# Kernel optimization log

Measured on AMD Instinct MI355X. Metric: run time of the kernel, lower is better.

Reference implementation:

```python
import jax, jax.numpy as jnp
import numpy as np

WS = 8          # window size
NH = 12         # num heads
DEPTH = 2       # blocks: W-MSA, SW-MSA
EPS = 1e-6
N = WS * WS     # tokens per window


def _rel_index():
    c = np.stack(np.meshgrid(np.arange(WS), np.arange(WS), indexing='ij')).reshape(2, -1)
    rel = (c[:, :, None] - c[:, None, :]).transpose(1, 2, 0)
    rel[:, :, 0] += WS - 1
    rel[:, :, 1] += WS - 1
    rel[:, :, 0] *= 2 * WS - 1
    return rel.sum(-1)  # [N, N] int

REL_IDX = jnp.asarray(_rel_index())


def _shift_mask(H, W, shift):
    # static (numpy) construction, H/W/shift are Python ints
    img = np.zeros((H, W))
    cnt = 0
    for hs in (slice(0, -WS), slice(-WS, -shift), slice(-shift, None)):
        for wsl in (slice(0, -WS), slice(-WS, -shift), slice(-shift, None)):
            img[hs, wsl] = cnt
            cnt += 1
    win = img.reshape(H // WS, WS, W // WS, WS).transpose(0, 2, 1, 3).reshape(-1, N)
    diff = win[:, None, :] - win[:, :, None]
    return jnp.asarray(np.where(diff != 0, -100.0, 0.0), jnp.float32)  # [nW, N, N]


def _ln(x):
    m = x.mean(-1, keepdims=True)
    v = ((x - m) ** 2).mean(-1, keepdims=True)
    return (x - m) * jax.lax.rsqrt(v + EPS)


def _block(x, H, W, emb, p, shift):
    qkv_w, qkv_b, proj_w, proj_b, ff1_w, ff1_b, ff2_w, ff2_b, ada_w, ada_b, bias_table = p
    B, L, C = x.shape
    hd = C // NH
    ada = jax.nn.silu(emb) @ ada_w.T + ada_b  # [B, 6C]
    sh_sa, sc_sa, g_sa, sh_ff, sc_ff, g_ff = jnp.split(ada, 6, axis=-1)
    h = _ln(x) * (1.0 + sc_sa[:, None]) + sh_sa[:, None]
    h = h.reshape(B, H, W, C)
    if shift > 0:
        h = jnp.roll(h, (-shift, -shift), (1, 2))
    # window partition -> [B*nW, N, C]
    win = h.reshape(B, H // WS, WS, W // WS, WS, C).transpose(0, 1, 3, 2, 4, 5).reshape(-1, N, C)
    B_ = win.shape[0]
    qkv = (win @ qkv_w.T + qkv_b).reshape(B_, N, 3, NH, hd)
    q, k, v = qkv[:, :, 0], qkv[:, :, 1], qkv[:, :, 2]
    attn = jnp.einsum('bnhd,bmhd->bhnm', q, k) * (hd ** -0.5)
    bias = bias_table[REL_IDX]  # [N, N, NH]
    attn = attn + bias.transpose(2, 0, 1)[None]
    if shift > 0:
        mask = _shift_mask(H, W, shift)  # [nW, N, N]
        nW = mask.shape[0]
        attn = (attn.reshape(B, nW, NH, N, N) + mask[None, :, None]).reshape(B_, NH, N, N)
    attn = jax.nn.softmax(attn, axis=-1)
    out = jnp.einsum('bhnm,bmhd->bnhd', attn, v).reshape(B_, N, C)
    out = out @ proj_w.T + proj_b
    # window reverse
    h = out.reshape(B, H // WS, W // WS, WS, WS, C).transpose(0, 1, 3, 2, 4, 5).reshape(B, H, W, C)
    if shift > 0:
        h = jnp.roll(h, (shift, shift), (1, 2))
    x = x + g_sa[:, None] * h.reshape(B, L, C)
    h2 = _ln(x) * (1.0 + sc_ff[:, None]) + sh_ff[:, None]
    ff = jax.nn.gelu(h2 @ ff1_w.T + ff1_b, approximate=False) @ ff2_w.T + ff2_b
    return x + g_ff[:, None] * ff


def _forward(x, emb, H, W, params):
    for i in range(DEPTH):
        p = tuple(a[i] for a in params)
        x = _block(x, H, W, emb, p, 0 if i % 2 == 0 else WS // 2)
    return x


def setup_inputs() -> dict:
    key = jax.random.key(0)
    ks = jax.random.split(key, 16)
    C, E, FF = 384, 384, 4 * 384
    B, H, W = 8, 64, 64
    p = lambda k, shape: jax.random.normal(k, shape, jnp.float32) * 0.02
    return {
        'x': jax.random.normal(ks[0], (B, H * W, C), jnp.float32),
        'H': H,
        'W': W,
        'emb': jax.random.normal(ks[1], (B, E), jnp.float32),
        'qkv_w': p(ks[2], (DEPTH, 3 * C, C)),
        'qkv_b': p(ks[3], (DEPTH, 3 * C)),
        'proj_w': p(ks[4], (DEPTH, C, C)),
        'proj_b': p(ks[5], (DEPTH, C)),
        'ff1_w': p(ks[6], (DEPTH, FF, C)),
        'ff1_b': p(ks[7], (DEPTH, FF)),
        'ff2_w': p(ks[8], (DEPTH, C, FF)),
        'ff2_b': p(ks[9], (DEPTH, C)),
        'ada_w': p(ks[10], (DEPTH, 6 * C, E)),
        'ada_b': p(ks[11], (DEPTH, 6 * C)),
        'bias_table': p(ks[12], (DEPTH, (2 * WS - 1) ** 2, NH)),
    }


def reference(x, H, W, emb, qkv_w, qkv_b, proj_w, proj_b, ff1_w, ff1_b, ff2_w, ff2_b, ada_w, ada_b, bias_table):
    params = (qkv_w, qkv_b, proj_w, proj_b, ff1_w, ff1_b, ff2_w, ff2_b, ada_w, ada_b, bias_table)
    return _forward(x, emb, H, W, params)
```

## Files before the change

kernel.cpp:

```cpp
#include <hip/hip_runtime.h>

typedef __bf16 bf16_t;
typedef bf16_t bf16x8 __attribute__((ext_vector_type(8)));
typedef float f32x4 __attribute__((ext_vector_type(4)));

#define EPI_STORE 0
#define EPI_GELU 1
#define EPI_RES_WIN 2
#define EPI_RES_ID 3

__device__ __forceinline__ float bf2f(unsigned short u) {
    union { unsigned int i; float f; } x; x.i = ((unsigned int)u) << 16; return x.f;
}
__device__ __forceinline__ unsigned short f2bf(float f) {
    union { float f; unsigned int u; } x; x.f = f;
    unsigned int u = x.u;
    return (unsigned short)((u + 0x7fffu + ((u >> 16) & 1u)) >> 16);
}

__device__ __forceinline__ void async_cp16(const unsigned short* g, unsigned short* l) {
    __builtin_amdgcn_global_load_lds(
        (const __attribute__((address_space(1))) unsigned int*)g,
        (__attribute__((address_space(3))) unsigned int*)l, 16, 0, 0);
}

__device__ __forceinline__ int map_win(int m, int shift) {
    int n = m & 63, w = m >> 6;
    int b = w >> 6, ww = w & 63;
    int hh = ((ww >> 3) * 8 + (n >> 3) + shift) & 63;
    int wc = ((ww & 7) * 8 + (n & 7) + shift) & 63;
    return (b << 12) + (hh << 6) + wc;
}


__global__ void f2bf_kernel(const float* __restrict__ in,
                            unsigned short* __restrict__ out, int n) {
    int i = blockIdx.x * 256 + threadIdx.x;
    if (i < n) out[i] = f2bf(in[i]);
}

__global__ void silu_kernel(const float* __restrict__ emb,
                            float* __restrict__ out, int n) {
    int i = blockIdx.x * 256 + threadIdx.x;
    if (i < n) { float e = emb[i]; out[i] = e / (1.0f + expf(-e)); }
}

__global__ __launch_bounds__(64) void ada_kernel(
    const float* __restrict__ se,
    const float* __restrict__ ada_w,
    const float* __restrict__ ada_b,
    float* __restrict__ ada_out)
{
    int j = blockIdx.x;
    int layer = blockIdx.y;
    int t = threadIdx.x;
    const float* wr = ada_w + ((long)layer * 2304 + j) * 384;
    float w[6];
#pragma unroll
    for (int q = 0; q < 6; q++) w[q] = wr[t + 64 * q];
    float bias = ada_b[layer * 2304 + j];
    for (int b = 0; b < 8; b++) {
        float p = 0.f;
#pragma unroll
        for (int q = 0; q < 6; q++) p += se[b * 384 + t + 64 * q] * w[q];
#pragma unroll
        for (int o = 32; o > 0; o >>= 1) p += __shfl_xor(p, o);
        if (t == 0) ada_out[((long)layer * 8 + b) * 2304 + j] = p + bias;
    }
}

__global__ __launch_bounds__(256) void ln_mod_kernel(
    const float* __restrict__ x, const float* __restrict__ ada,
    unsigned short* __restrict__ h, int sh_off, int sc_off)
{
    int row = blockIdx.x * 4 + (threadIdx.x >> 6);
    int b = row >> 12;
    int t = threadIdx.x & 63;
    const float* xr = x + (long)row * 384;
    float v[6];
    float s = 0.f;
#pragma unroll
    for (int j = 0; j < 6; j++) { v[j] = xr[t + 64 * j]; s += v[j]; }
#pragma unroll
    for (int o = 32; o > 0; o >>= 1) s += __shfl_xor(s, o);
    float mean = s * (1.0f / 384.0f);
    float s2 = 0.f;
#pragma unroll
    for (int j = 0; j < 6; j++) { float d = v[j] - mean; s2 += d * d; }
#pragma unroll
    for (int o = 32; o > 0; o >>= 1) s2 += __shfl_xor(s2, o);
    float rstd = rsqrtf(s2 * (1.0f / 384.0f) + 1e-6f);
    const float* adab = ada + (long)b * 2304;
#pragma unroll
    for (int j = 0; j < 6; j++) {
        int c = t + 64 * j;
        float val = (v[j] - mean) * rstd * (1.0f + adab[sc_off + c]) + adab[sh_off + c];
        h[(long)row * 384 + c] = f2bf(val);
    }
}


template <int EPI, bool GATHER, bool RESINIT>
__global__ __launch_bounds__(256) void gemm128(
    const unsigned short* __restrict__ A,
    const unsigned short* __restrict__ W,
    const float* __restrict__ bias,
    unsigned short* __restrict__ out,
    float* __restrict__ xres,
    const float* __restrict__ xbase,
    const float* __restrict__ gvec,
    int M, int N, int K, int shift)
{
    __shared__ __align__(16) unsigned short As[128 * 32];
    __shared__ __align__(16) unsigned short Bs[128 * 32];

    const int tid = threadIdx.x;
    const int wv = tid >> 6, lane = tid & 63;
    const int m0 = blockIdx.y * 128, n0 = blockIdx.x * 128;

    const int srow = wv * 32 + (lane >> 2);
    const int scol = (lane & 3) * 8;
    const long asrc0 = GATHER ? (long)map_win(m0 + srow, shift) : (long)(m0 + srow);
    const long asrc1 = GATHER ? (long)map_win(m0 + srow + 16, shift) : (long)(m0 + srow + 16);
    const unsigned short* ag0 = A + asrc0 * K + scol;
    const unsigned short* ag1 = A + asrc1 * K + scol;
    const unsigned short* bg0 = W + (long)(n0 + srow) * K + scol;
    const unsigned short* bg1 = W + (long)(n0 + srow + 16) * K + scol;
    unsigned short* al0 = As + wv * 1024;
    unsigned short* al1 = As + wv * 1024 + 512;
    unsigned short* bl0 = Bs + wv * 1024;
    unsigned short* bl1 = Bs + wv * 1024 + 512;

    const int wm = (wv >> 1) * 64, wn = (wv & 1) * 64;
    const int l16 = lane & 15, quad = lane >> 4;

    f32x4 acc[4][4] = {};

    for (int k0 = 0; k0 < K; k0 += 32) {
        async_cp16(ag0 + k0, al0);
        async_cp16(ag1 + k0, al1);
        async_cp16(bg0 + k0, bl0);
        async_cp16(bg1 + k0, bl1);
        __syncthreads();

        bf16x8 af[4], bfr[4];
#pragma unroll
        for (int i = 0; i < 4; i++)
            af[i] = *(const bf16x8*)&As[(wm + i * 16 + l16) * 32 + quad * 8];
#pragma unroll
        for (int i = 0; i < 4; i++)
            bfr[i] = *(const bf16x8*)&Bs[(wn + i * 16 + l16) * 32 + quad * 8];
#pragma unroll
        for (int i = 0; i < 4; i++)
#pragma unroll
            for (int j = 0; j < 4; j++)
                acc[i][j] = __builtin_amdgcn_mfma_f32_16x16x32_bf16(af[i], bfr[j], acc[i][j], 0, 0, 0);
        __syncthreads();
    }

#pragma unroll
    for (int i = 0; i < 4; i++) {
#pragma unroll
        for (int j = 0; j < 4; j++) {
            int col = n0 + wn + j * 16 + l16;
            float bv = bias[col];
#pragma unroll
            for (int r = 0; r < 4; r++) {
                int row = m0 + wm + i * 16 + quad * 4 + r;
                float v = acc[i][j][r] + bv;
                if constexpr (EPI == EPI_STORE) {
                    out[(long)row * N + col] = f2bf(v);
                } else if constexpr (EPI == EPI_GELU) {
                    v = 0.5f * v * (1.0f + erff(v * 0.70710678118f));
                    out[(long)row * N + col] = f2bf(v);
                } else {
                    long dst = (EPI == EPI_RES_WIN) ? (long)map_win(row, shift) : (long)row;
                    int b = (int)(dst >> 12);
                    float g = gvec[(long)b * 2304 + col];
                    if constexpr (RESINIT)
                        xres[dst * 384 + col] = xbase[dst * 384 + col] + g * v;
                    else
                        xres[dst * 384 + col] += g * v;
                }
            }
        }
    }
}


__device__ __forceinline__ int reg3(int p) { return (p < 56) ? 0 : ((p < 60) ? 1 : 2); }

__global__ __launch_bounds__(256) void attn_kernel(
    const unsigned short* __restrict__ qkv,
    const float* __restrict__ bias_table,
    unsigned short* __restrict__ out,
    int shift)
{
    __shared__ unsigned short Pl[4][64 * 68];
    __shared__ unsigned short VTl[4][32 * 68];

    const int wv = threadIdx.x >> 6, lane = threadIdx.x & 63;
    const int head = blockIdx.x * 4 + wv;
    const int win = blockIdx.y;
    const int l16 = lane & 15, quad = lane >> 4;

    unsigned short* P = Pl[wv];
    unsigned short* vt = VTl[wv];

    const long base = (long)win * 64 * 1152 + head * 32;

    bf16x8 qf[4], kf[4];
#pragma unroll
    for (int i = 0; i < 4; i++) {
        qf[i] = *(const bf16x8*)&qkv[base + (long)(i * 16 + l16) * 1152 + quad * 8];
        kf[i] = *(const bf16x8*)&qkv[base + 384 + (long)(i * 16 + l16) * 1152 + quad * 8];
    }
    {
        const uint4* vp = (const uint4*)&qkv[base + 768 + (long)lane * 1152];
#pragma unroll
        for (int c4 = 0; c4 < 4; c4++) {
            uint4 v = vp[c4];
            unsigned int u[4] = {v.x, v.y, v.z, v.w};
#pragma unroll
            for (int e = 0; e < 4; e++) {
                vt[(c4 * 8 + e * 2) * 68 + lane]     = (unsigned short)(u[e] & 0xffffu);
                vt[(c4 * 8 + e * 2 + 1) * 68 + lane] = (unsigned short)(u[e] >> 16);
            }
        }
    }

    f32x4 sacc[4][4] = {};
#pragma unroll
    for (int i = 0; i < 4; i++)
#pragma unroll
        for (int j = 0; j < 4; j++)
            sacc[i][j] = __builtin_amdgcn_mfma_f32_16x16x32_bf16(qf[i], kf[j], sacc[i][j], 0, 0, 0);

    const float scale = 0.17677669529663687f;
    const int ww = win & 63, wi = ww >> 3, wj = ww & 7;

#pragma unroll
    for (int i = 0; i < 4; i++) {
#pragma unroll
        for (int r = 0; r < 4; r++) {
            int n = i * 16 + quad * 4 + r;
            int nr = n >> 3, nc = n & 7;
            int labq = (shift > 0) ? reg3(wi * 8 + nr) * 3 + reg3(wj * 8 + nc) : 0;
            float v[4];
#pragma unroll
            for (int j = 0; j < 4; j++) {
                int m = j * 16 + l16;
                int mr = m >> 3, mc = m & 7;
                float s = sacc[i][j][r] * scale +
                          bias_table[((nr - mr + 7) * 15 + (nc - mc + 7)) * 12 + head];
                if (shift > 0) {
                    int labm = reg3(wi * 8 + mr) * 3 + reg3(wj * 8 + mc);
                    if (labm != labq) s -= 100.0f;
                }
                v[j] = s;
            }
            float mx = fmaxf(fmaxf(v[0], v[1]), fmaxf(v[2], v[3]));
#pragma unroll
            for (int o = 1; o < 16; o <<= 1) mx = fmaxf(mx, __shfl_xor(mx, o));
            float sum = 0.f;
#pragma unroll
            for (int j = 0; j < 4; j++) { v[j] = __expf(v[j] - mx); sum += v[j]; }
#pragma unroll
            for (int o = 1; o < 16; o <<= 1) sum += __shfl_xor(sum, o);
            float inv = 1.0f / sum;
#pragma unroll
            for (int j = 0; j < 4; j++)
                P[n * 68 + j * 16 + l16] = f2bf(v[j] * inv);
        }
    }
    __syncthreads();

    f32x4 oacc[4][2] = {};
#pragma unroll
    for (int kt = 0; kt < 2; kt++) {
        bf16x8 pf[4], vf[2];
#pragma unroll
        for (int i = 0; i < 4; i++)
            pf[i] = *(const bf16x8*)&P[(i * 16 + l16) * 68 + kt * 32 + quad * 8];
#pragma unroll
        for (int jt = 0; jt < 2; jt++)
            vf[jt] = *(const bf16x8*)&vt[(jt * 16 + l16) * 68 + kt * 32 + quad * 8];
#pragma unroll
        for (int i = 0; i < 4; i++)
#pragma unroll
            for (int jt = 0; jt < 2; jt++)
                oacc[i][jt] = __builtin_amdgcn_mfma_f32_16x16x32_bf16(pf[i], vf[jt], oacc[i][jt], 0, 0, 0);
    }

#pragma unroll
    for (int i = 0; i < 4; i++)
#pragma unroll
        for (int jt = 0; jt < 2; jt++)
#pragma unroll
            for (int r = 0; r < 4; r++) {
                int row = i * 16 + quad * 4 + r;
                int col = jt * 16 + l16;
                out[((long)win * 64 + row) * 384 + head * 32 + col] = f2bf(oacc[i][jt][r]);
            }
}


extern "C" void kernel_launch(void* const* d_in, const int* in_sizes, int n_in,
                              void* d_out, int out_size, void* d_ws, size_t ws_size,
                              hipStream_t stream) {
    const float* x_in   = (const float*)d_in[0];
    const float* emb    = (const float*)d_in[3];
    const float* qkv_w  = (const float*)d_in[4];
    const float* qkv_b  = (const float*)d_in[5];
    const float* proj_w = (const float*)d_in[6];
    const float* proj_b = (const float*)d_in[7];
    const float* ff1_w  = (const float*)d_in[8];
    const float* ff1_b  = (const float*)d_in[9];
    const float* ff2_w  = (const float*)d_in[10];
    const float* ff2_b  = (const float*)d_in[11];
    const float* ada_w  = (const float*)d_in[12];
    const float* ada_b  = (const float*)d_in[13];
    const float* bias_t = (const float*)d_in[14];

    char* ws = (char*)d_ws;
    unsigned short* h_buf   = (unsigned short*)ws;
    unsigned short* big_buf = (unsigned short*)(ws + 25165824);
    unsigned short* wqkv    = (unsigned short*)(ws + 125829120);
    unsigned short* wproj   = (unsigned short*)(ws + 127598592);
    unsigned short* wff1    = (unsigned short*)(ws + 128188416);
    unsigned short* wff2    = (unsigned short*)(ws + 130547712);
    float*          ada_out = (float*)(ws + 132907008);
    float*          se      = (float*)(ws + 133054464);

    float* x_acc = (float*)d_out;

    const int M = 32768;

    f2bf_kernel<<<(884736 + 255) / 256, 256, 0, stream>>>(qkv_w, wqkv, 884736);
    f2bf_kernel<<<(294912 + 255) / 256, 256, 0, stream>>>(proj_w, wproj, 294912);
    f2bf_kernel<<<(1179648 + 255) / 256, 256, 0, stream>>>(ff1_w, wff1, 1179648);
    f2bf_kernel<<<(1179648 + 255) / 256, 256, 0, stream>>>(ff2_w, wff2, 1179648);

    silu_kernel<<<(3072 + 255) / 256, 256, 0, stream>>>(emb, se, 3072);
    ada_kernel<<<dim3(2304, 2), 64, 0, stream>>>(se, ada_w, ada_b, ada_out);

    for (int layer = 0; layer < 2; layer++) {
        const int shift = layer ? 4 : 0;
        const float* ada_l = ada_out + (long)layer * 8 * 2304;

        ln_mod_kernel<<<M / 4, 256, 0, stream>>>(layer == 0 ? x_in : x_acc,
                                                 ada_l, h_buf, 0, 384);

        gemm128<EPI_STORE, true, false><<<dim3(9, 256), 256, 0, stream>>>(
            h_buf, wqkv + (long)layer * 1152 * 384, qkv_b + layer * 1152,
            big_buf, nullptr, nullptr, nullptr, M, 1152, 384, shift);

        attn_kernel<<<dim3(3, 512), 256, 0, stream>>>(
            big_buf, bias_t + layer * 225 * 12, h_buf, shift);

        if (layer == 0) {
            gemm128<EPI_RES_WIN, false, true><<<dim3(3, 256), 256, 0, stream>>>(
                h_buf, wproj, proj_b,
                nullptr, x_acc, x_in, ada_l + 768, M, 384, 384, shift);
        } else {
            gemm128<EPI_RES_WIN, false, false><<<dim3(3, 256), 256, 0, stream>>>(
                h_buf, wproj + (long)384 * 384, proj_b + 384,
                nullptr, x_acc, nullptr, ada_l + 768, M, 384, 384, shift);
        }

        ln_mod_kernel<<<M / 4, 256, 0, stream>>>(x_acc, ada_l, h_buf, 1152, 1536);

        gemm128<EPI_GELU, false, false><<<dim3(12, 256), 256, 0, stream>>>(
            h_buf, wff1 + (long)layer * 1536 * 384, ff1_b + layer * 1536,
            big_buf, nullptr, nullptr, nullptr, M, 1536, 384, 0);

        gemm128<EPI_RES_ID, false, false><<<dim3(3, 256), 256, 0, stream>>>(
            big_buf, wff2 + (long)layer * 384 * 1536, ff2_b + layer * 384,
            nullptr, x_acc, nullptr, ada_l + 1920, M, 384, 1536, 0);
    }
}
```

Measured before the change: 794.8 us.

## Deepen GEMM K-tile to 64 with XOR-swizzled LDS, fast GELU and bf16 cast

Doubles the GEMM K-step to 64 so each shared-memory load and barrier pair covers twice the MFMA work. LDS tiles use an XOR swizzle on 16-byte chunks to avoid bank conflicts on the fragment reads. The erf-based GELU is replaced by a tanh-approximation written with __expf, and the manual round-to-nearest bf16 conversion becomes a native __bf16 cast. The epilogue hoists bias loads per column and reorders the loops so each row's address is computed once. The tanh approximation changes numerics slightly relative to exact erf GELU, and the larger tiles double LDS use per block, which may lower occupancy.

```diff
diff --git a/kernel.cpp b/kernel.cpp
--- a/kernel.cpp
+++ b/kernel.cpp
@@ -13,9 +13,11 @@
     union { unsigned int i; float f; } x; x.i = ((unsigned int)u) << 16; return x.f;
 }
 __device__ __forceinline__ unsigned short f2bf(float f) {
-    union { float f; unsigned int u; } x; x.f = f;
-    unsigned int u = x.u;
-    return (unsigned short)((u + 0x7fffu + ((u >> 16) & 1u)) >> 16);
+    union { __bf16 h; unsigned short u; } c; c.h = (__bf16)f; return c.u;
+}
+__device__ __forceinline__ float gelu_f(float v) {
+    float u = v * (0.7978845608f + 0.0356774081f * v * v);
+    return v / (1.0f + __expf(-2.0f * u));
 }
 
 __device__ __forceinline__ void async_cp16(const unsigned short* g, unsigned short* l) {
@@ -111,76 +113,88 @@
     const float* __restrict__ gvec,
     int M, int N, int K, int shift)
 {
-    __shared__ __align__(16) unsigned short As[128 * 32];
-    __shared__ __align__(16) unsigned short Bs[128 * 32];
+    __shared__ __align__(16) unsigned short As[128 * 64];
+    __shared__ __align__(16) unsigned short Bs[128 * 64];
 
     const int tid = threadIdx.x;
     const int wv = tid >> 6, lane = tid & 63;
     const int m0 = blockIdx.y * 128, n0 = blockIdx.x * 128;
 
-    const int srow = wv * 32 + (lane >> 2);
-    const int scol = (lane & 3) * 8;
-    const long asrc0 = GATHER ? (long)map_win(m0 + srow, shift) : (long)(m0 + srow);
-    const long asrc1 = GATHER ? (long)map_win(m0 + srow + 16, shift) : (long)(m0 + srow + 16);
-    const unsigned short* ag0 = A + asrc0 * K + scol;
-    const unsigned short* ag1 = A + asrc1 * K + scol;
-    const unsigned short* bg0 = W + (long)(n0 + srow) * K + scol;
-    const unsigned short* bg1 = W + (long)(n0 + srow + 16) * K + scol;
-    unsigned short* al0 = As + wv * 1024;
-    unsigned short* al1 = As + wv * 1024 + 512;
-    unsigned short* bl0 = Bs + wv * 1024;
-    unsigned short* bl1 = Bs + wv * 1024 + 512;
+    const int r8 = lane >> 3;
+    const int cofs = ((lane & 7) ^ r8) * 8;
+    long arow[4], brow[4];
+#pragma unroll
+    for (int t = 0; t < 4; t++) {
+        int rl = wv * 32 + t * 8 + r8;
+        arow[t] = GATHER ? (long)map_win(m0 + rl, shift) : (long)(m0 + rl);
+        brow[t] = (long)(n0 + rl);
+    }
 
     const int wm = (wv >> 1) * 64, wn = (wv & 1) * 64;
     const int l16 = lane & 15, quad = lane >> 4;
+    const int swz = l16 & 7;
 
     f32x4 acc[4][4] = {};
 
-    for (int k0 = 0; k0 < K; k0 += 32) {
-        async_cp16(ag0 + k0, al0);
-        async_cp16(ag1 + k0, al1);
-        async_cp16(bg0 + k0, bl0);
-        async_cp16(bg1 + k0, bl1);
+    for (int k0 = 0; k0 < K; k0 += 64) {
+#pragma unroll
+        for (int t = 0; t < 4; t++) {
+            async_cp16(A + arow[t] * K + k0 + cofs, As + (wv * 32 + t * 8) * 64);
+            async_cp16(W + brow[t] * K + k0 + cofs, Bs + (wv * 32 + t * 8) * 64);
+        }
         __syncthreads();
 
-        bf16x8 af[4], bfr[4];
-#pragma unroll
-        for (int i = 0; i < 4; i++)
-            af[i] = *(const bf16x8*)&As[(wm + i * 16 + l16) * 32 + quad * 8];
-#pragma unroll
-        for (int i = 0; i < 4; i++)
-            bfr[i] = *(const bf16x8*)&Bs[(wn + i * 16 + l16) * 32 + quad * 8];
-#pragma unroll
-        for (int i = 0; i < 4; i++)
+#pragma unroll
+        for (int kk = 0; kk < 2; kk++) {
+            bf16x8 af[4], bfr[4];
+#pragma unroll
+            for (int i = 0; i < 4; i++)
+                af[i] = *(const bf16x8*)&As[(wm + i * 16 + l16) * 64 +
+                                            (((kk * 4 + quad) ^ swz) * 8)];
 #pragma unroll
             for (int j = 0; j < 4; j++)
-                acc[i][j] = __builtin_amdgcn_mfma_f32_16x16x32_bf16(af[i], bfr[j], acc[i][j], 0, 0, 0);
+                bfr[j] = *(const bf16x8*)&Bs[(wn + j * 16 + l16) * 64 +
+                                             (((kk * 4 + quad) ^ swz) * 8)];
+#pragma unroll
+            for (int i = 0; i < 4; i++)
+#pragma unroll
+                for (int j = 0; j < 4; j++)
+                    acc[i][j] = __builtin_amdgcn_mfma_f32_16x16x32_bf16(af[i], bfr[j], acc[i][j], 0, 0, 0);
+        }
         __syncthreads();
     }
 
+    float bv[4];
+#pragma unroll
+    for (int j = 0; j < 4; j++) bv[j] = bias[n0 + wn + j * 16 + l16];
+
 #pragma unroll
     for (int i = 0; i < 4; i++) {
 #pragma unroll
-        for (int j = 0; j < 4; j++) {
-            int col = n0 + wn + j * 16 + l16;
-            float bv = bias[col];
-#pragma unroll
-            for (int r = 0; r < 4; r++) {
-                int row = m0 + wm + i * 16 + quad * 4 + r;
-                float v = acc[i][j][r] + bv;
-                if constexpr (EPI == EPI_STORE) {
-                    out[(long)row * N + col] = f2bf(v);
-                } else if constexpr (EPI == EPI_GELU) {
-                    v = 0.5f * v * (1.0f + erff(v * 0.70710678118f));
-                    out[(long)row * N + col] = f2bf(v);
-                } else {
-                    long dst = (EPI == EPI_RES_WIN) ? (long)map_win(row, shift) : (long)row;
-                    int b = (int)(dst >> 12);
-                    float g = gvec[(long)b * 2304 + col];
-                    if constexpr (RESINIT)
-                        xres[dst * 384 + col] = xbase[dst * 384 + col] + g * v;
-                    else
-                        xres[dst * 384 + col] += g * v;
+        for (int r = 0; r < 4; r++) {
+            int row = m0 + wm + i * 16 + quad * 4 + r;
+            if constexpr (EPI == EPI_STORE || EPI == EPI_GELU) {
+                unsigned short* orow = out + (long)row * N + n0 + wn + l16;
+#pragma unroll
+                for (int j = 0; j < 4; j++) {
+                    float v = acc[i][j][r] + bv[j];
+                    if constexpr (EPI == EPI_GELU) v = gelu_f(v);
+                    orow[j * 16] = f2bf(v);
+                }
+            } else {
+                long dst = (EPI == EPI_RES_WIN) ? (long)map_win(row, shift) : (long)row;
+                int b = (int)(dst >> 12);
+                float* xrow = xres + dst * 384 + n0 + wn + l16;
+                const float* grow = gvec + (long)b * 2304 + n0 + wn + l16;
+#pragma unroll
+                for (int j = 0; j < 4; j++) {
+                    float v = acc[i][j][r] + bv[j];
+                    if constexpr (RESINIT) {
+                        const float* xbrow = xbase + dst * 384 + n0 + wn + l16;
+                        xrow[j * 16] = xbrow[j * 16] + grow[j * 16] * v;
+                    } else {
+                        xrow[j * 16] += grow[j * 16] * v;
+                    }
                 }
             }
         }
```

Result: faster. 771.7 us (-2.9%).
